# Performance work log

Hardware: AMD Instinct MI355X
Metric: run time of the kernel (lower is better)

Reference implementation:

```python
import jax, jax.numpy as jnp
import numpy as np

# ---- module constants (from init_kwargs) ----
N_DIM = 2                      # n: latent dim (len(active_dims))
T_STEPS = 100                  # t: linspace(0,1,t) integration grid
M_PER_DIM = 12                 # m = [12,12] HSGP basis per dim
C_FACTOR = 1.5                 # c: HSGP domain expansion factor
X_EXTENT = 3.0                 # data extent (x0 ~ N(0,1) lives in [-3,3])
L_BOUND = C_FACTOR * X_EXTENT  # HSGP half-domain length L = c*S
D_COMPS = N_DIM * (N_DIM + 1) // 2  # d = 3 metric components

# eigen-index grid over all dim combinations: [M_TOTAL, n]
_J = np.stack(np.meshgrid(*[np.arange(1, M_PER_DIM + 1)] * N_DIM, indexing='ij'), -1)
J = jnp.asarray(_J.reshape(-1, N_DIM).astype(np.float32))
M_TOTAL = J.shape[0]
_r, _c = np.triu_indices(N_DIM)
ROWS, COLS = jnp.asarray(_r), jnp.asarray(_c)

# explicit Adams-Bashforth coefficients (orders 1..4), newest derivative first
AB_COEFFS = jnp.array([
    [1.0, 0.0, 0.0, 0.0],
    [1.5, -0.5, 0.0, 0.0],
    [23.0/12.0, -16.0/12.0, 5.0/12.0, 0.0],
    [55.0/24.0, -59.0/24.0, 37.0/24.0, -9.0/24.0]], dtype=jnp.float32)


def hsgp_features(x, ls, alpha):
    """HSGP ExpQuad linearized basis phi(x) and its spatial derivative dphi.
    x: [B, n] -> phi: [B, M], dphi: [B, M, n]."""
    w = jnp.pi * J / (2.0 * L_BOUND)                  # [M, n] per-dim frequencies
    arg = w[None] * (x[:, None, :] + L_BOUND)         # [B, M, n]
    s, c = jnp.sin(arg), jnp.cos(arg)
    norm = L_BOUND ** (-0.5 * N_DIM)
    phi = norm * jnp.prod(s, axis=-1)                 # [B, M]
    dcols = []
    for i in range(N_DIM):                            # structural loop over n=2 dims
        p = w[None, :, i] * c[:, :, i]
        for j2 in range(N_DIM):
            if j2 != i:
                p = p * s[:, :, j2]
        dcols.append(norm * p)
    dphi = jnp.stack(dcols, axis=-1)                  # [B, M, n]
    # ExpQuad spectral density sqrt weights
    S = (alpha ** 2) * ((2.0 * jnp.pi) ** (0.5 * N_DIM)) * jnp.prod(ls) \
        * jnp.exp(-0.5 * jnp.sum((ls ** 2)[None] * w ** 2, axis=-1))  # [M]
    sq = jnp.sqrt(S)
    return phi * sq[None], dphi * sq[None, :, None]


def geodesic_rhs(y, beta, ls, alpha):
    """geomstats-style geodesic equation: y = stack([x, v]) -> stack([v, a]),
    a^k = -Gamma^k_{ij} v^i v^j with GP-parameterized Christoffels."""
    x, v = y[0], y[1]                                 # [B, n]
    B = x.shape[0]
    phi, dphi = hsgp_features(x, ls, alpha)
    f = phi @ beta.T                                  # [B, d] metric components
    df = jnp.einsum('bmi,dm->bdi', dphi, beta)        # [B, d, n] their derivatives
    G = jnp.zeros((B, N_DIM, N_DIM), x.dtype)
    G = G.at[:, ROWS, COLS].set(f).at[:, COLS, ROWS].set(f)
    G = G + jnp.eye(N_DIM, dtype=x.dtype)             # identity offset keeps G invertible
    D = jnp.zeros((B, N_DIM, N_DIM, N_DIM), x.dtype)  # D[b,l,j,i] = d_i g_{lj}
    D = D.at[:, ROWS, COLS, :].set(df).at[:, COLS, ROWS, :].set(df)
    Ginv = jnp.linalg.inv(G)
    # term[b,l,i,j] = d_i g_{lj} + d_j g_{li} - d_l g_{ij}
    term = jnp.transpose(D, (0, 1, 3, 2)) + D - jnp.transpose(D, (0, 3, 1, 2))
    Gam = 0.5 * jnp.einsum('bkl,blij->bkij', Ginv, term)
    acc = -jnp.einsum('bkij,bi,bj->bk', Gam, v, v)
    return jnp.stack([v, acc])


def adams_integrate(y0, beta, ls, alpha, rhs):
    """Fixed-grid explicit Adams (order<=4, lower-order startup) over linspace(0,1,t)."""
    h = jnp.float32(1.0 / (T_STEPS - 1))
    hist0 = jnp.zeros((4,) + y0.shape, y0.dtype)
    def step(carry, idx):
        y, hist = carry
        fcur = rhs(y, beta, ls, alpha)
        hist = jnp.concatenate([fcur[None], hist[:-1]], axis=0)  # newest first
        coef = AB_COEFFS[jnp.minimum(idx, 3)]
        y_next = y + h * jnp.tensordot(coef, hist, axes=1)
        return (y_next, hist), y_next
    _, ys = jax.lax.scan(step, (y0, hist0), jnp.arange(T_STEPS - 1))
    return jnp.concatenate([y0[None], ys], axis=0)    # [t, 2, B, n]


def setup_inputs():
    key = jax.random.key(0)
    k1, k2, k3, k4 = jax.random.split(key, 4)
    B = 50000
    x0 = jax.random.normal(k1, (B, N_DIM), jnp.float32)
    v0 = 0.2 * jax.random.normal(k2, (B, N_DIM), jnp.float32)
    beta = 0.05 * jax.random.normal(k3, (D_COMPS, M_TOTAL), jnp.float32)
    ls = 0.3 + 0.5 * jax.random.uniform(k4, (N_DIM,), jnp.float32)
    alpha = jnp.float32(1.0)
    return {"x0": x0, "v0": v0, "beta": beta, "ls": ls, "alpha": alpha}


def reference(x0, v0, beta, ls, alpha):
    y0 = jnp.stack([x0, v0])                          # [2, B, n]
    return adams_integrate(y0, beta, ls, alpha, geodesic_rhs)
```

## Files before the change

### kernel.cpp

```cpp
#include <hip/hip_runtime.h>
#include <math.h>

typedef _Float16 h4 __attribute__((ext_vector_type(4)));
typedef float    f4 __attribute__((ext_vector_type(4)));

namespace {
constexpr float LB = 4.5f;
constexpr float WF = (float)M_PI / (2.0f * LB);
}

__global__ void setup_A_kernel(const float* __restrict__ beta,
                               const float* __restrict__ ls,
                               const float* __restrict__ alpha,
                               _Float16* __restrict__ A) {
    int idx = blockIdx.x * blockDim.x + threadIdx.x;
    if (idx >= 768) return;
    int d = idx >> 8;
    int l = (idx >> 2) & 63;
    int t = idx & 3;
    int r = l & 15;
    int k = ((l >> 4) << 2) + t;
    float val = 0.0f;
    if (r < 12 && k < 12) {
        float w0 = WF * (float)(r + 1);
        float w1 = WF * (float)(k + 1);
        float l0 = ls[0], l1 = ls[1], al = alpha[0];
        float S = al * al * (2.0f * (float)M_PI) * l0 * l1 *
                  expf(-0.5f * (l0 * l0 * w0 * w0 + l1 * l1 * w1 * w1));
        val = beta[d * 144 + r * 12 + k] * sqrtf(S) * (1.0f / LB);
    }
    A[idx] = (_Float16)val;
}

__device__ __forceinline__ void trig4(float th, float mb, float* s, float* c) {
    float s1 = __sinf(th), c1 = __cosf(th);
    float sb = __sinf(mb * th), cb = __cosf(mb * th);
    s[0] = sb; c[0] = cb;
    #pragma unroll
    for (int t = 1; t < 4; ++t) {
        s[t] = fmaf(s[t - 1], c1,  c[t - 1] * s1);
        c[t] = fmaf(c[t - 1], c1, -(s[t - 1] * s1));
    }
}

__global__ __launch_bounds__(256)
void geo_kernel(const float* __restrict__ xg, const float* __restrict__ vg,
                const _Float16* Ag ,
                float* __restrict__ out, int B)
{
    int lane = threadIdx.x & 63;
    int wave = (blockIdx.x * 256 + threadIdx.x) >> 6;
    int ebase = wave << 4;
    if (ebase >= B) return;
    int g = lane >> 4;
    int e = ebase + (lane & 15);
    if (e >= B) e = B - 1;

    union U8 { uint2 u; h4 h; };
    const uint2* Au = reinterpret_cast<const uint2*>(Ag);
    U8 a0, a1, a2;
    a0.u = Au[0 * 64 + lane];
    a1.u = Au[1 * 64 + lane];
    a2.u = Au[2 * 64 + lane];
    asm volatile("" ::: "memory");
    h4 A0 = a0.h, A1 = a1.h, A2 = a2.h;

    float mb = (float)(4 * g + 1);
    float Wm[4];
    #pragma unroll
    for (int t = 0; t < 4; ++t) Wm[t] = WF * (mb + (float)t);

    float2 xv = reinterpret_cast<const float2*>(xg)[e];
    float2 vv2 = reinterpret_cast<const float2*>(vg)[e];
    float x0 = xv.x, x1 = xv.y, v0 = vv2.x, v1 = vv2.y;

    unsigned off = 4u * ((((unsigned)(g >> 1) * (unsigned)B) + (unsigned)e) * 2u
                         + (unsigned)(g & 1));
    const unsigned stride = 16u * (unsigned)B;
    char* outc = reinterpret_cast<char*>(out);
    {
        float sval = (g & 2) ? ((g & 1) ? v1 : v0) : ((g & 1) ? x1 : x0);
        *reinterpret_cast<float*>(outc + off) = sval;
    }

    float h1x = 0.f, h2x = 0.f, h3x = 0.f, h1y = 0.f, h2y = 0.f, h3y = 0.f;
    float g1x = 0.f, g2x = 0.f, g3x = 0.f, g1y = 0.f, g2y = 0.f, g3y = 0.f;
    const float h = 1.0f / 99.0f;

    auto STEP = [&](float c0, float c1c, float c2c, float c3c) {
        float s0v[4], c0v[4], s1v[4], c1v[4], wc0[4];
        trig4(WF * (x0 + LB), mb, s0v, c0v);
        trig4(WF * (x1 + LB), mb, s1v, c1v);
        #pragma unroll
        for (int t = 0; t < 4; ++t) wc0[t] = Wm[t] * c0v[t];

        h4 bs, bc;
        #pragma unroll
        for (int t = 0; t < 4; ++t) {
            bs[t] = (_Float16)s1v[t];
            bc[t] = (_Float16)(Wm[t] * c1v[t]);
        }

        f4 z = {0.f, 0.f, 0.f, 0.f};
        f4 u0 = __builtin_amdgcn_mfma_f32_16x16x16f16(A0, bs, z, 0, 0, 0);
        f4 u1 = __builtin_amdgcn_mfma_f32_16x16x16f16(A1, bs, z, 0, 0, 0);
        f4 u2 = __builtin_amdgcn_mfma_f32_16x16x16f16(A2, bs, z, 0, 0, 0);
        f4 w0 = __builtin_amdgcn_mfma_f32_16x16x16f16(A0, bc, z, 0, 0, 0);
        f4 w1 = __builtin_amdgcn_mfma_f32_16x16x16f16(A1, bc, z, 0, 0, 0);
        f4 w2 = __builtin_amdgcn_mfma_f32_16x16x16f16(A2, bc, z, 0, 0, 0);

        float f0 = 0.f, f1 = 0.f, f2 = 0.f;
        float dA0 = 0.f, dA1 = 0.f, dA2 = 0.f;
        float dB0 = 0.f, dB1 = 0.f, dB2 = 0.f;
        #pragma unroll
        for (int t = 0; t < 4; ++t) {
            float sA = s0v[t], cA = wc0[t];
            f0  = fmaf(sA, u0[t], f0);   dA0 = fmaf(cA, u0[t], dA0);
            f1  = fmaf(sA, u1[t], f1);   dA1 = fmaf(cA, u1[t], dA1);
            f2  = fmaf(sA, u2[t], f2);   dA2 = fmaf(cA, u2[t], dA2);
            dB0 = fmaf(sA, w0[t], dB0);
            dB1 = fmaf(sA, w1[t], dB1);
            dB2 = fmaf(sA, w2[t], dB2);
        }

        float vv00 = v0 * v0, vv01 = v0 * v1, vv11 = v1 * v1;
        float q0p = dA0 * vv00 + 2.0f * dB0 * vv01 + fmaf(2.0f, dB1, -dA2) * vv11;
        float q1p = fmaf(2.0f, dA1, -dB0) * vv00 + 2.0f * dA2 * vv01 + dB2 * vv11;

        f0  += __shfl_xor(f0, 16);  f0  += __shfl_xor(f0, 32);
        f1  += __shfl_xor(f1, 16);  f1  += __shfl_xor(f1, 32);
        f2  += __shfl_xor(f2, 16);  f2  += __shfl_xor(f2, 32);
        q0p += __shfl_xor(q0p, 16); q0p += __shfl_xor(q0p, 32);
        q1p += __shfl_xor(q1p, 16); q1p += __shfl_xor(q1p, 32);

        float G00 = f0 + 1.0f, G01 = f1, G11 = f2 + 1.0f;
        float det = fmaf(G00, G11, -(G01 * G01));
        float rdet = __builtin_amdgcn_rcpf(det);
        float a0v = -0.5f * rdet * fmaf(G11, q0p, -(G01 * q1p));
        float a1v = -0.5f * rdet * fmaf(G00, q1p, -(G01 * q0p));

        float dx0 = fmaf(c0, v0, fmaf(c1c, h1x, fmaf(c2c, h2x, c3c * h3x)));
        float dx1 = fmaf(c0, v1, fmaf(c1c, h1y, fmaf(c2c, h2y, c3c * h3y)));
        float dv0 = fmaf(c0, a0v, fmaf(c1c, g1x, fmaf(c2c, g2x, c3c * g3x)));
        float dv1 = fmaf(c0, a1v, fmaf(c1c, g1y, fmaf(c2c, g2y, c3c * g3y)));
        h3x = h2x; h2x = h1x; h1x = v0;  h3y = h2y; h2y = h1y; h1y = v1;
        g3x = g2x; g2x = g1x; g1x = a0v; g3y = g2y; g2y = g1y; g1y = a1v;
        x0 = fmaf(h, dx0, x0); x1 = fmaf(h, dx1, x1);
        v0 = fmaf(h, dv0, v0); v1 = fmaf(h, dv1, v1);

        off += stride;
        float sval = (g & 2) ? ((g & 1) ? v1 : v0) : ((g & 1) ? x1 : x0);
        *reinterpret_cast<float*>(outc + off) = sval;
    };

    STEP(1.0f, 0.0f, 0.0f, 0.0f);
    STEP(1.5f, -0.5f, 0.0f, 0.0f);
    STEP(23.0f / 12.0f, -16.0f / 12.0f, 5.0f / 12.0f, 0.0f);
    #pragma unroll 2
    for (int t = 3; t < 99; ++t)
        STEP(55.0f / 24.0f, -59.0f / 24.0f, 37.0f / 24.0f, -9.0f / 24.0f);
}

extern "C" void kernel_launch(void* const* d_in, const int* in_sizes, int n_in,
                              void* d_out, int out_size, void* d_ws, size_t ws_size,
                              hipStream_t stream) {
    const float* x0    = (const float*)d_in[0];
    const float* v0    = (const float*)d_in[1];
    const float* beta  = (const float*)d_in[2];
    const float* ls    = (const float*)d_in[3];
    const float* alpha = (const float*)d_in[4];
    float* out = (float*)d_out;
    _Float16* A = (_Float16*)d_ws;

    int B = in_sizes[0] / 2;

    hipLaunchKernelGGL(setup_A_kernel, dim3(12), dim3(64), 0, stream,
                       beta, ls, alpha, A);

    int waves = (B + 15) / 16;
    int grid  = (waves + 3) / 4;
    hipLaunchKernelGGL(geo_kernel, dim3(grid), dim3(256), 0, stream,
                       x0, v0, A, out, B);
}
```

Baseline: 139.2 us.

## Replace shuffle reductions with ones-matrix MFMA sums and use single-wave blocks

The cross-lane reduction over the four lane groups moves from shuffle-xor pairs onto nine extra 16x16x16 f16 MFMAs that multiply a matrix of ones by packed elementwise products. These replace ten DPP/shuffle ops per step but add nine MFMAs plus fp16 packing, and the summed terms are now rounded to half precision, which can cost accuracy. The f16 packing uses the cvt_pkrtz intrinsic, blocks shrink to one 64-thread wave, and the main time loop unroll rises to 4. The q products are now computed after the reduction rather than before it, which changes the arithmetic order.

```diff
diff --git a/kernel.cpp b/kernel.cpp
--- a/kernel.cpp
+++ b/kernel.cpp
@@ -2,6 +2,7 @@
 #include <math.h>
 
 typedef _Float16 h4 __attribute__((ext_vector_type(4)));
+typedef _Float16 h2 __attribute__((ext_vector_type(2)));
 typedef float    f4 __attribute__((ext_vector_type(4)));
 
 namespace {
@@ -43,14 +44,19 @@
     }
 }
 
-__global__ __launch_bounds__(256)
+__device__ __forceinline__ h4 pack4(float a, float b, float c, float d) {
+    h2 lo = __builtin_bit_cast(h2, __builtin_amdgcn_cvt_pkrtz(a, b));
+    h2 hi = __builtin_bit_cast(h2, __builtin_amdgcn_cvt_pkrtz(c, d));
+    return __builtin_shufflevector(lo, hi, 0, 1, 2, 3);
+}
+
+__global__ __launch_bounds__(64)
 void geo_kernel(const float* __restrict__ xg, const float* __restrict__ vg,
                 const _Float16* Ag ,
                 float* __restrict__ out, int B)
 {
-    int lane = threadIdx.x & 63;
-    int wave = (blockIdx.x * 256 + threadIdx.x) >> 6;
-    int ebase = wave << 4;
+    int lane = threadIdx.x;
+    int ebase = blockIdx.x << 4;
     if (ebase >= B) return;
     int g = lane >> 4;
     int e = ebase + (lane & 15);
@@ -64,6 +70,7 @@
     a2.u = Au[2 * 64 + lane];
     asm volatile("" ::: "memory");
     h4 A0 = a0.h, A1 = a1.h, A2 = a2.h;
+    h4 ONES = {(_Float16)1.0f, (_Float16)1.0f, (_Float16)1.0f, (_Float16)1.0f};
 
     float mb = (float)(4 * g + 1);
     float Wm[4];
@@ -94,12 +101,9 @@
         #pragma unroll
         for (int t = 0; t < 4; ++t) wc0[t] = Wm[t] * c0v[t];
 
-        h4 bs, bc;
-        #pragma unroll
-        for (int t = 0; t < 4; ++t) {
-            bs[t] = (_Float16)s1v[t];
-            bc[t] = (_Float16)(Wm[t] * c1v[t]);
-        }
+        h4 bs = pack4(s1v[0], s1v[1], s1v[2], s1v[3]);
+        h4 bc = pack4(Wm[0] * c1v[0], Wm[1] * c1v[1],
+                      Wm[2] * c1v[2], Wm[3] * c1v[3]);
 
         f4 z = {0.f, 0.f, 0.f, 0.f};
         f4 u0 = __builtin_amdgcn_mfma_f32_16x16x16f16(A0, bs, z, 0, 0, 0);
@@ -109,29 +113,33 @@
         f4 w1 = __builtin_amdgcn_mfma_f32_16x16x16f16(A1, bc, z, 0, 0, 0);
         f4 w2 = __builtin_amdgcn_mfma_f32_16x16x16f16(A2, bc, z, 0, 0, 0);
 
-        float f0 = 0.f, f1 = 0.f, f2 = 0.f;
-        float dA0 = 0.f, dA1 = 0.f, dA2 = 0.f;
-        float dB0 = 0.f, dB1 = 0.f, dB2 = 0.f;
-        #pragma unroll
-        for (int t = 0; t < 4; ++t) {
-            float sA = s0v[t], cA = wc0[t];
-            f0  = fmaf(sA, u0[t], f0);   dA0 = fmaf(cA, u0[t], dA0);
-            f1  = fmaf(sA, u1[t], f1);   dA1 = fmaf(cA, u1[t], dA1);
-            f2  = fmaf(sA, u2[t], f2);   dA2 = fmaf(cA, u2[t], dA2);
-            dB0 = fmaf(sA, w0[t], dB0);
-            dB1 = fmaf(sA, w1[t], dB1);
-            dB2 = fmaf(sA, w2[t], dB2);
-        }
+        h4 Pf0 = pack4(s0v[0]*u0[0], s0v[1]*u0[1], s0v[2]*u0[2], s0v[3]*u0[3]);
+        h4 Pf1 = pack4(s0v[0]*u1[0], s0v[1]*u1[1], s0v[2]*u1[2], s0v[3]*u1[3]);
+        h4 Pf2 = pack4(s0v[0]*u2[0], s0v[1]*u2[1], s0v[2]*u2[2], s0v[3]*u2[3]);
+        h4 Pa0 = pack4(wc0[0]*u0[0], wc0[1]*u0[1], wc0[2]*u0[2], wc0[3]*u0[3]);
+        h4 Pa1 = pack4(wc0[0]*u1[0], wc0[1]*u1[1], wc0[2]*u1[2], wc0[3]*u1[3]);
+        h4 Pa2 = pack4(wc0[0]*u2[0], wc0[1]*u2[1], wc0[2]*u2[2], wc0[3]*u2[3]);
+        h4 Pb0 = pack4(s0v[0]*w0[0], s0v[1]*w0[1], s0v[2]*w0[2], s0v[3]*w0[3]);
+        h4 Pb1 = pack4(s0v[0]*w1[0], s0v[1]*w1[1], s0v[2]*w1[2], s0v[3]*w1[3]);
+        h4 Pb2 = pack4(s0v[0]*w2[0], s0v[1]*w2[1], s0v[2]*w2[2], s0v[3]*w2[3]);
+
+        f4 F0  = __builtin_amdgcn_mfma_f32_16x16x16f16(ONES, Pf0, z, 0, 0, 0);
+        f4 F1  = __builtin_amdgcn_mfma_f32_16x16x16f16(ONES, Pf1, z, 0, 0, 0);
+        f4 F2  = __builtin_amdgcn_mfma_f32_16x16x16f16(ONES, Pf2, z, 0, 0, 0);
+        f4 DA0 = __builtin_amdgcn_mfma_f32_16x16x16f16(ONES, Pa0, z, 0, 0, 0);
+        f4 DA1 = __builtin_amdgcn_mfma_f32_16x16x16f16(ONES, Pa1, z, 0, 0, 0);
+        f4 DA2 = __builtin_amdgcn_mfma_f32_16x16x16f16(ONES, Pa2, z, 0, 0, 0);
+        f4 DB0 = __builtin_amdgcn_mfma_f32_16x16x16f16(ONES, Pb0, z, 0, 0, 0);
+        f4 DB1 = __builtin_amdgcn_mfma_f32_16x16x16f16(ONES, Pb1, z, 0, 0, 0);
+        f4 DB2 = __builtin_amdgcn_mfma_f32_16x16x16f16(ONES, Pb2, z, 0, 0, 0);
+
+        float f0 = F0[0], f1 = F1[0], f2 = F2[0];
+        float dA0 = DA0[0], dA1 = DA1[0], dA2 = DA2[0];
+        float dB0 = DB0[0], dB1 = DB1[0], dB2 = DB2[0];
 
         float vv00 = v0 * v0, vv01 = v0 * v1, vv11 = v1 * v1;
         float q0p = dA0 * vv00 + 2.0f * dB0 * vv01 + fmaf(2.0f, dB1, -dA2) * vv11;
         float q1p = fmaf(2.0f, dA1, -dB0) * vv00 + 2.0f * dA2 * vv01 + dB2 * vv11;
-
-        f0  += __shfl_xor(f0, 16);  f0  += __shfl_xor(f0, 32);
-        f1  += __shfl_xor(f1, 16);  f1  += __shfl_xor(f1, 32);
-        f2  += __shfl_xor(f2, 16);  f2  += __shfl_xor(f2, 32);
-        q0p += __shfl_xor(q0p, 16); q0p += __shfl_xor(q0p, 32);
-        q1p += __shfl_xor(q1p, 16); q1p += __shfl_xor(q1p, 32);
 
         float G00 = f0 + 1.0f, G01 = f1, G11 = f2 + 1.0f;
         float det = fmaf(G00, G11, -(G01 * G01));
@@ -156,7 +164,7 @@
     STEP(1.0f, 0.0f, 0.0f, 0.0f);
     STEP(1.5f, -0.5f, 0.0f, 0.0f);
     STEP(23.0f / 12.0f, -16.0f / 12.0f, 5.0f / 12.0f, 0.0f);
-    #pragma unroll 2
+    #pragma unroll 4
     for (int t = 3; t < 99; ++t)
         STEP(55.0f / 24.0f, -59.0f / 24.0f, 37.0f / 24.0f, -9.0f / 24.0f);
 }
@@ -177,8 +185,7 @@
     hipLaunchKernelGGL(setup_A_kernel, dim3(12), dim3(64), 0, stream,
                        beta, ls, alpha, A);
 
-    int waves = (B + 15) / 16;
-    int grid  = (waves + 3) / 4;
-    hipLaunchKernelGGL(geo_kernel, dim3(grid), dim3(256), 0, stream,
+    int grid = (B + 15) / 16;
+    hipLaunchKernelGGL(geo_kernel, dim3(grid), dim3(64), 0, stream,
                        x0, v0, A, out, B);
 }
```

Measured after the change: 145.4 us. 4.4% more time.
